# Kernel tuning notes

Measured on AMD Instinct MI355X. Metric: run time of the kernel, lower is better.

The kernel has to match this reference:

```python
import jax, jax.numpy as jnp
import numpy as np

N, B, NPG = 65536, 512, 128      # total nodes, graphs, nodes per graph
E, EPG = 524288, 1024            # total edges, edges per graph
D, R, L = 64, 16, 3              # emb_dim, num relations, encoder layers
PHI = 0.1
EPS_VAR = 1e-5


def _mean_std(x):
    # torch.var is unbiased (ddof=1); keep last-dim stats per row
    m = jnp.mean(x, axis=-1, keepdims=True)
    s = jnp.sqrt(jnp.var(x, axis=-1, ddof=1, keepdims=True) + EPS_VAR)
    return m, s


def _rgcn_encode(feat, Wrel, Wself, b, src, dst, etype, edge_w):
    """L-layer relational GCN. Returns (last_h [N,D], repr [N,L,D])."""
    h = feat
    reps = []
    for l in range(L):
        hr = jnp.einsum('nd,rdk->nrk', h, Wrel[l])        # [N,R,D]
        msg = hr[src, etype]                               # [E,D] per-edge typed transform
        msg = msg * edge_w[:, None]
        agg = jax.ops.segment_sum(msg, dst, num_segments=N)
        deg = jax.ops.segment_sum(edge_w, dst, num_segments=N)
        h = jax.nn.relu(h @ Wself[l] + agg / jnp.clip(deg, 1.0)[:, None] + b[l])
        reps.append(h)
    return h, jnp.stack(reps, axis=1)


def _pool(rep, node_gid):
    # mean_nodes over 'repr': graphs have fixed NPG nodes
    s = jax.ops.segment_sum(rep.reshape(N, L * D), node_gid, num_segments=B)
    return (s / NPG).reshape(B, L, D)


def full_forward(feat, rel_feat, rel_proj_W, rel_proj_b, rgcn_Wrel, rgcn_Wself,
                 rgcn_b, enc_W_mean, enc_W_std, dec_Wh, dec_bh, dec_Wt, dec_bt,
                 dec_Wr, dec_br, fc_W, fc_b, eps,
                 src, dst, etype, aug_src, aug_dst, aug_etype, node_gid, rel_labels):
    ones_e = jnp.ones((E,), feat.dtype)
    # relation encoder + projection
    emb_rel = jax.nn.relu(rel_feat @ rel_proj_W + rel_proj_b)          # [R,D]
    # encode original and augmented graphs
    x, rep_g = _rgcn_encode(feat, rgcn_Wrel, rgcn_Wself, rgcn_b, src, dst, etype, ones_e)
    g_out = _pool(rep_g, node_gid)
    aug_x, rep_aug = _rgcn_encode(feat, rgcn_Wrel, rgcn_Wself, rgcn_b, aug_src, aug_dst, aug_etype, ones_e)
    aug_g_out = _pool(rep_aug, node_gid)
    # AdaIn style transfer (args.interp == False)
    mc, sc = _mean_std(x)
    ms, ss = _mean_std(aug_x)
    style_applied = ss * ((x - mc) / sc) + ms
    # VAE reparameterization
    z_mean = style_applied @ enc_W_mean
    z_std = style_applied @ enc_W_std
    z = z_mean + jnp.sqrt(jnp.exp(z_std)) * eps
    # decoder: edge-level DistMult scoring -> edge mask
    head_e = jax.nn.relu(z[src] @ dec_Wh + dec_bh)                     # [E,D]
    tail_e = jax.nn.relu(z[dst] @ dec_Wt + dec_bt)
    rel_e = jax.nn.relu(emb_rel[etype] @ dec_Wr + dec_br)
    logit = jnp.sum(head_e * rel_e * tail_e, axis=-1)                  # [E]
    mask = (logit >= 0.5).astype(feat.dtype)
    # root edge (edge_ids(0,1)) = first edge of each graph, forced kept
    mask = mask.at[jnp.arange(B) * EPG].set(1.0)
    # re-encode reconstructed (masked) graph with original features
    x_recon, rep_recon = _rgcn_encode(feat, rgcn_Wrel, rgcn_Wself, rgcn_b, src, dst, etype, mask)
    recon_g_out = _pool(rep_recon, node_gid)
    # head node (id==1) = node 0 of each graph; tail (id==2) = node 1
    head_ids = jnp.arange(B) * NPG
    tail_ids = head_ids + 1
    g_rep = jnp.concatenate([
        recon_g_out.reshape(B, L * D),
        rep_recon[head_ids].reshape(B, L * D),
        rep_recon[tail_ids].reshape(B, L * D),
        emb_rel[rel_labels],
    ], axis=1)                                                          # [B, 3*L*D + D]
    output = g_rep @ fc_W + fc_b                                        # [B,1]
    # reconstruction + style losses, summed over layers
    mse_per_layer = jnp.mean((rep_recon - rep_g) ** 2, axis=(0, 2))     # [L]
    mr, sr = _mean_std(rep_recon.transpose(1, 0, 2))                    # [L,N,1]
    mg, sg = _mean_std(rep_g.transpose(1, 0, 2))
    style_per_layer = jnp.mean((mr - mg) ** 2, axis=(1, 2)) + jnp.mean((sr - sg) ** 2, axis=(1, 2))
    loss = jnp.sum(mse_per_layer) + PHI * jnp.sum(style_per_layer)
    return output, g_out, aug_g_out, loss


def setup_inputs() -> dict:
    key = jax.random.key(0)
    ks = jax.random.split(key, 28)
    egid = jnp.arange(E, dtype=jnp.int32) // EPG
    node_gid = jnp.arange(N, dtype=jnp.int32) // NPG
    mk_edges = lambda k1, k2: (egid * NPG + jax.random.randint(k1, (E,), 0, NPG, jnp.int32),
                               egid * NPG + jax.random.randint(k2, (E,), 0, NPG, jnp.int32))
    src, dst = mk_edges(ks[0], ks[1])
    aug_src, aug_dst = mk_edges(ks[2], ks[3])
    g = lambda i, shape, s=0.05: (jax.random.normal(ks[i], shape, jnp.float32) * s)
    return {
        'feat': g(4, (N, D), 1.0),
        'rel_feat': g(5, (R, 64), 1.0),
        'rel_proj_W': g(6, (64, D)),
        'rel_proj_b': jnp.zeros((D,), jnp.float32),
        'rgcn_Wrel': g(7, (L, R, D, D)),
        'rgcn_Wself': g(8, (L, D, D)),
        'rgcn_b': jnp.zeros((L, D), jnp.float32),
        'enc_W_mean': g(9, (D, D)),
        'enc_W_std': g(10, (D, D)),
        'dec_Wh': g(11, (D, D), 0.1),
        'dec_bh': jnp.zeros((D,), jnp.float32),
        'dec_Wt': g(12, (D, D), 0.1),
        'dec_bt': jnp.zeros((D,), jnp.float32),
        'dec_Wr': g(13, (D, D), 0.1),
        'dec_br': jnp.zeros((D,), jnp.float32),
        'fc_W': g(14, (3 * L * D + D, 1)),
        'fc_b': jnp.zeros((1,), jnp.float32),
        'eps': g(15, (N, D), 1.0),
        'src': src, 'dst': dst,
        'etype': jax.random.randint(ks[16], (E,), 0, R, jnp.int32),
        'aug_src': aug_src, 'aug_dst': aug_dst,
        'aug_etype': jax.random.randint(ks[17], (E,), 0, R, jnp.int32),
        'node_gid': node_gid,
        'rel_labels': jax.random.randint(ks[18], (B,), 0, R, jnp.int32),
    }


def reference(feat, rel_feat, rel_proj_W, rel_proj_b, rgcn_Wrel, rgcn_Wself,
              rgcn_b, enc_W_mean, enc_W_std, dec_Wh, dec_bh, dec_Wt, dec_bt,
              dec_Wr, dec_br, fc_W, fc_b, eps,
              src, dst, etype, aug_src, aug_dst, aug_etype, node_gid, rel_labels):
    return full_forward(feat, rel_feat, rel_proj_W, rel_proj_b, rgcn_Wrel, rgcn_Wself,
                        rgcn_b, enc_W_mean, enc_W_std, dec_Wh, dec_bh, dec_Wt, dec_bt,
                        dec_Wr, dec_br, fc_W, fc_b, eps,
                        src, dst, etype, aug_src, aug_dst, aug_etype, node_gid, rel_labels)
```

## Files before the change

### kernel.cpp

```cpp
#include <hip/hip_runtime.h>
#include <hip/hip_bf16.h>

typedef __attribute__((ext_vector_type(8))) short bf16x8;
typedef __attribute__((ext_vector_type(4))) float f32x4;

#define NPG  128
#define EPG  1024
#define BG   512
#define NT   512
#define NW   8
#define PHI  0.1f
#define EPSV 1e-5f
#define SB   72
#define SF   65

#define OUT_G    512
#define OUT_AUG  98816
#define OUT_LOSS 197120
#define WS_EMB   0
#define WS_RELE  1024
#define WS_REPG  2048

__device__ __forceinline__ unsigned short f2bf(float x) {
  __hip_bfloat16 h = __float2bfloat16(x);
  return *reinterpret_cast<unsigned short*>(&h);
}
__device__ __forceinline__ float bf2f(unsigned short u) {
  __hip_bfloat16 h = *reinterpret_cast<__hip_bfloat16*>(&u);
  return __bfloat162float(h);
}
__device__ __forceinline__ void split_write(unsigned short* hh, unsigned short* hl,
                                            int idx, float x) {
  unsigned short hi = f2bf(x);
  hh[idx] = hi;
  hl[idx] = f2bf(x - bf2f(hi));
}

#define LOAD_BF(Wp, ctn, ks, bhv, blv)                                         \
  {                                                                            \
    bf16x8 h_, l_;                                                             \
    _Pragma("unroll") for (int j_ = 0; j_ < 8; j_++) {                         \
      float w_ = (Wp)[((ks) * 32 + kg * 8 + j_) * 64 + (ctn) * 16 + n];        \
      unsigned short hi_ = f2bf(w_);                                           \
      h_[j_] = (short)hi_;                                                     \
      l_[j_] = (short)f2bf(w_ - bf2f(hi_));                                    \
    }                                                                          \
    bhv = h_;                                                                  \
    blv = l_;                                                                  \
  }

__device__ __forceinline__ f32x4 mfma3(bf16x8 a0h, bf16x8 a1h, bf16x8 a0l, bf16x8 a1l,
                                       bf16x8 b0h, bf16x8 b1h, bf16x8 b0l, bf16x8 b1l,
                                       f32x4 acc) {
  acc = __builtin_amdgcn_mfma_f32_16x16x32_bf16(a0h, b0h, acc, 0, 0, 0);
  acc = __builtin_amdgcn_mfma_f32_16x16x32_bf16(a1h, b1h, acc, 0, 0, 0);
  acc = __builtin_amdgcn_mfma_f32_16x16x32_bf16(a0h, b0l, acc, 0, 0, 0);
  acc = __builtin_amdgcn_mfma_f32_16x16x32_bf16(a1h, b1l, acc, 0, 0, 0);
  acc = __builtin_amdgcn_mfma_f32_16x16x32_bf16(a0l, b0h, acc, 0, 0, 0);
  acc = __builtin_amdgcn_mfma_f32_16x16x32_bf16(a1l, b1h, acc, 0, 0, 0);
  return acc;
}

__global__ __launch_bounds__(256) void k_prologue(
    const float* __restrict__ rel_feat, const float* __restrict__ rpW,
    const float* __restrict__ rpb, const float* __restrict__ dWr,
    const float* __restrict__ dbr, float* __restrict__ ws, float* __restrict__ out) {
  __shared__ float emb[1024];
  int tid = threadIdx.x;
  for (int idx = tid; idx < 1024; idx += 256) {
    int r = idx >> 6, j = idx & 63;
    float s = rpb[j];
    for (int k = 0; k < 64; k++) s = fmaf(rel_feat[r * 64 + k], rpW[k * 64 + j], s);
    s = fmaxf(s, 0.f);
    emb[idx] = s;
    ws[WS_EMB + idx] = s;
  }
  __syncthreads();
  for (int idx = tid; idx < 1024; idx += 256) {
    int r = idx >> 6, j = idx & 63;
    float s = dbr[j];
    for (int k = 0; k < 64; k++) s = fmaf(emb[r * 64 + k], dWr[k * 64 + j], s);
    ws[WS_RELE + idx] = fmaxf(s, 0.f);
  }
  if (tid == 0) out[OUT_LOSS] = 0.f;
}

__device__ void build_elist(unsigned* elist, int* cnt, int* offs, int* asg, int* wload,
                            float* dinv, const unsigned* maskbits, int useMask,
                            const int* __restrict__ et_a, const int* __restrict__ src_a,
                            const int* __restrict__ dst_a, int ge, int gn, int tid) {
  if (tid < 16) cnt[tid] = 0;
  if (tid >= 128 && tid < 256) dinv[tid - 128] = 0.f;
  __syncthreads();
  for (int i = tid; i < EPG; i += NT) {
    int keep = useMask ? (int)((maskbits[i >> 5] >> (i & 31)) & 1u) : 1;
    if (keep) {
      atomicAdd(&cnt[et_a[ge + i]], 1);
      atomicAdd(&dinv[dst_a[ge + i] - gn], 1.f);
    }
  }
  __syncthreads();
  if (tid == 0) {
    int o = 0;
    for (int r = 0; r < 16; r++) { offs[r] = o; o += (cnt[r] + 15) & ~15; }
    offs[16] = o;
    for (int w = 0; w < NW; w++) wload[w] = 0;
    unsigned used = 0;
    for (int s = 0; s < 16; s++) {
      int best = 0, bc = -1;
      for (int r = 0; r < 16; r++)
        if (!((used >> r) & 1) && cnt[r] > bc) { bc = cnt[r]; best = r; }
      used |= 1u << best;
      int bw = 0;
      for (int w = 1; w < NW; w++) if (wload[w] < wload[bw]) bw = w;
      asg[best] = bw;
      wload[bw] += (bc + 15) & ~15;
    }
  }
  if (tid >= 128 && tid < 256) {
    int v = tid - 128;
    dinv[v] = 1.0f / fmaxf(dinv[v], 1.0f);
  }
  __syncthreads();
  int total = offs[16];
  for (int s = tid; s < total; s += NT) elist[s] = 128u;
  if (tid < 16) cnt[tid] = offs[tid];
  __syncthreads();
  for (int i = tid; i < EPG; i += NT) {
    int keep = useMask ? (int)((maskbits[i >> 5] >> (i & 31)) & 1u) : 1;
    if (keep) {
      int r = et_a[ge + i];
      int pos = atomicAdd(&cnt[r], 1);
      elist[pos] = ((unsigned)(src_a[ge + i] - gn) << 8) | (unsigned)(dst_a[ge + i] - gn);
    }
  }
  __syncthreads();
}

__device__ void rgcn_layer_mfma(unsigned short* hh, unsigned short* hl, float* hf32,
                                const float* dinv, const unsigned* elist,
                                const int* offs, const int* asg,
                                const float* __restrict__ Wl,
                                const float* __restrict__ Wsl,
                                const float* __restrict__ bl, int tid) {
  int lane = tid & 63, wave = tid >> 6;
  int n = lane & 15, kg = lane >> 4;
  for (int i = tid; i < NPG * SF; i += NT) hf32[i] = 0.f;
  __syncthreads();
  for (int r = 0; r < 16; r++) {
    if (asg[r] != wave) continue;
    int base = offs[r], end = offs[r + 1];
    if (base >= end) continue;
    const float* __restrict__ W = Wl + (r << 12);
#pragma unroll 1
    for (int ch = 0; ch < 2; ch++) {
      bf16x8 bh00, bh01, bl00, bl01, bh10, bh11, bl10, bl11;
      LOAD_BF(W, ch * 2 + 0, 0, bh00, bl00);
      LOAD_BF(W, ch * 2 + 0, 1, bh01, bl01);
      LOAD_BF(W, ch * 2 + 1, 0, bh10, bl10);
      LOAD_BF(W, ch * 2 + 1, 1, bh11, bl11);
      for (int tb = base; tb < end; tb += 16) {
        int srow = (int)(elist[tb + n] >> 8);
        const unsigned short* rh = hh + srow * SB;
        const unsigned short* rl = hl + srow * SB;
        bf16x8 a0h = *(const bf16x8*)(rh + kg * 8);
        bf16x8 a1h = *(const bf16x8*)(rh + 32 + kg * 8);
        bf16x8 a0l = *(const bf16x8*)(rl + kg * 8);
        bf16x8 a1l = *(const bf16x8*)(rl + 32 + kg * 8);
        f32x4 acc0 = {0.f, 0.f, 0.f, 0.f}, acc1 = {0.f, 0.f, 0.f, 0.f};
        acc0 = mfma3(a0h, a1h, a0l, a1l, bh00, bh01, bl00, bl01, acc0);
        acc1 = mfma3(a0h, a1h, a0l, a1l, bh10, bh11, bl10, bl11, acc1);
#pragma unroll
        for (int i = 0; i < 4; i++) {
          int dst = (int)(elist[tb + kg * 4 + i] & 255u);
          if (dst < 128) {
            float* hp = hf32 + dst * SF + ch * 32 + n;
            atomicAdd(hp, acc0[i]);
            atomicAdd(hp + 16, acc1[i]);
          }
        }
      }
    }
  }
  __syncthreads();
  {
    const unsigned short* rh = hh + (wave * 16 + n) * SB;
    const unsigned short* rl = hl + (wave * 16 + n) * SB;
    bf16x8 a0h = *(const bf16x8*)(rh + kg * 8);
    bf16x8 a1h = *(const bf16x8*)(rh + 32 + kg * 8);
    bf16x8 a0l = *(const bf16x8*)(rl + kg * 8);
    bf16x8 a1l = *(const bf16x8*)(rl + 32 + kg * 8);
#pragma unroll 1
    for (int ch = 0; ch < 2; ch++) {
      bf16x8 bh00, bh01, bl00, bl01, bh10, bh11, bl10, bl11;
      LOAD_BF(Wsl, ch * 2 + 0, 0, bh00, bl00);
      LOAD_BF(Wsl, ch * 2 + 0, 1, bh01, bl01);
      LOAD_BF(Wsl, ch * 2 + 1, 0, bh10, bl10);
      LOAD_BF(Wsl, ch * 2 + 1, 1, bh11, bl11);
      f32x4 acc0 = {0.f, 0.f, 0.f, 0.f}, acc1 = {0.f, 0.f, 0.f, 0.f};
      acc0 = mfma3(a0h, a1h, a0l, a1l, bh00, bh01, bl00, bl01, acc0);
      acc1 = mfma3(a0h, a1h, a0l, a1l, bh10, bh11, bl10, bl11, acc1);
#pragma unroll
      for (int i = 0; i < 4; i++) {
        int node = wave * 16 + kg * 4 + i;
        float di = dinv[node];
#pragma unroll
        for (int c = 0; c < 2; c++) {
          int col = (ch * 2 + c) * 16 + n;
          float a = c ? acc1[i] : acc0[i];
          float v = a + hf32[node * SF + col] * di + bl[col];
          v = fmaxf(v, 0.f);
          hf32[node * SF + col] = v;
          split_write(hh, hl, node * SB + col, v);
        }
      }
    }
  }
  __syncthreads();
}

__device__ void dense_mfma(const unsigned short* ah, const unsigned short* al,
                           float* hf32, unsigned short* oh, unsigned short* ol,
                           const float* __restrict__ W, const float* __restrict__ bias,
                           int mode, const float* __restrict__ epsbuf, int gn, int tid) {
  int lane = tid & 63, wave = tid >> 6;
  int n = lane & 15, kg = lane >> 4;
  const unsigned short* rh = ah + (wave * 16 + n) * SB;
  const unsigned short* rl = al + (wave * 16 + n) * SB;
  bf16x8 a0h = *(const bf16x8*)(rh + kg * 8);
  bf16x8 a1h = *(const bf16x8*)(rh + 32 + kg * 8);
  bf16x8 a0l = *(const bf16x8*)(rl + kg * 8);
  bf16x8 a1l = *(const bf16x8*)(rl + 32 + kg * 8);
#pragma unroll 1
  for (int ch = 0; ch < 2; ch++) {
    bf16x8 bh00, bh01, bl00, bl01, bh10, bh11, bl10, bl11;
    LOAD_BF(W, ch * 2 + 0, 0, bh00, bl00);
    LOAD_BF(W, ch * 2 + 0, 1, bh01, bl01);
    LOAD_BF(W, ch * 2 + 1, 0, bh10, bl10);
    LOAD_BF(W, ch * 2 + 1, 1, bh11, bl11);
    f32x4 acc0 = {0.f, 0.f, 0.f, 0.f}, acc1 = {0.f, 0.f, 0.f, 0.f};
    acc0 = mfma3(a0h, a1h, a0l, a1l, bh00, bh01, bl00, bl01, acc0);
    acc1 = mfma3(a0h, a1h, a0l, a1l, bh10, bh11, bl10, bl11, acc1);
#pragma unroll
    for (int i = 0; i < 4; i++) {
      int node = wave * 16 + kg * 4 + i;
#pragma unroll
      for (int c = 0; c < 2; c++) {
        int col = (ch * 2 + c) * 16 + n;
        float a = c ? acc1[i] : acc0[i];
        if (mode == 0) {
          hf32[node * SF + col] = a;
        } else if (mode == 2) {
          hf32[node * SF + col] += sqrtf(expf(a)) * epsbuf[(gn + node) * 64 + col];
        } else {
          a = fmaxf(a + bias[col], 0.f);
          if (oh) split_write(oh, ol, node * SB + col, a);
          else hf32[node * SF + col] = a;
        }
      }
    }
  }
  __syncthreads();
}

__device__ void pool_sf(const float* hf32, float* red, float* dst, int tid) {
  int j = tid & 63, grp = tid >> 6;
  float s = 0.f;
  for (int v = grp * 16; v < grp * 16 + 16; v++) s += hf32[v * SF + j];
  red[tid] = s;
  __syncthreads();
  if (tid < 64) {
    float t = 0.f;
#pragma unroll
    for (int w = 0; w < NW; w++) t += red[w * 64 + tid];
    dst[tid] = t * (1.f / 128.f);
  }
  __syncthreads();
}

__global__ __launch_bounds__(NT, 2) void k_mega(
    const float* __restrict__ feat, const float* __restrict__ Wrel,
    const float* __restrict__ Wself, const float* __restrict__ bvec,
    const float* __restrict__ encWm, const float* __restrict__ encWs,
    const float* __restrict__ decWh, const float* __restrict__ dbh,
    const float* __restrict__ decWt, const float* __restrict__ dbt,
    const float* __restrict__ fcW, const float* __restrict__ fcb,
    const float* __restrict__ epsbuf,
    const int* __restrict__ srcA, const int* __restrict__ dstA, const int* __restrict__ etA,
    const int* __restrict__ asrcA, const int* __restrict__ adstA, const int* __restrict__ aetA,
    const int* __restrict__ rel_labels, float* __restrict__ ws, float* __restrict__ out) {
  __shared__ __align__(16) unsigned short hh[NPG * SB];
  __shared__ __align__(16) unsigned short hl[NPG * SB];
  __shared__ __align__(16) float hf32[NPG * SF];
  __shared__ __align__(16) unsigned elist[1280];
  __shared__ float dinv[NPG];
  __shared__ float red[NT];
  __shared__ float ht[384];
  __shared__ float rgout[192];
  __shared__ unsigned maskbits[EPG / 32];
  __shared__ int cnt[16], offs[17], asg[16], wload[NW];

  int g = blockIdx.x, tid = threadIdx.x;
  int gn = g * NPG, ge = g * EPG;
  float* repg = ws + WS_REPG;

  build_elist(elist, cnt, offs, asg, wload, dinv, maskbits, 0, etA, srcA, dstA, ge, gn, tid);
  for (int i = tid; i < 8192; i += NT)
    split_write(hh, hl, (i >> 6) * SB + (i & 63), feat[gn * 64 + i]);
  __syncthreads();
  for (int l = 0; l < 3; l++) {
    rgcn_layer_mfma(hh, hl, hf32, dinv, elist, offs, asg, Wrel + l * 65536,
                    Wself + l * 4096, bvec + l * 64, tid);
    for (int i = tid; i < 8192; i += NT)
      repg[(gn + (i >> 6)) * 192 + l * 64 + (i & 63)] = hf32[(i >> 6) * SF + (i & 63)];
    pool_sf(hf32, red, out + OUT_G + g * 192 + l * 64, tid);
  }
  build_elist(elist, cnt, offs, asg, wload, dinv, maskbits, 0, aetA, asrcA, adstA, ge, gn, tid);
  for (int i = tid; i < 8192; i += NT)
    split_write(hh, hl, (i >> 6) * SB + (i & 63), feat[gn * 64 + i]);
  __syncthreads();
  for (int l = 0; l < 3; l++) {
    rgcn_layer_mfma(hh, hl, hf32, dinv, elist, offs, asg, Wrel + l * 65536,
                    Wself + l * 4096, bvec + l * 64, tid);
    pool_sf(hf32, red, out + OUT_AUG + g * 192 + l * 64, tid);
  }
  if (tid < NPG) {
    int v = tid;
    float t1 = 0.f, t2 = 0.f;
    for (int jj = 0; jj < 64; jj++) {
      int j = (v + jj) & 63;
      float y = hf32[v * SF + j];
      t1 += y; t2 += y * y;
    }
    float ms = t1 * (1.f / 64.f);
    red[v] = ms;
    red[NPG + v] = sqrtf((t2 - 64.f * ms * ms) * (1.f / 63.f) + EPSV);
  }
  __syncthreads();
  for (int i = tid; i < 8192; i += NT)
    hf32[(i >> 6) * SF + (i & 63)] = repg[(gn + (i >> 6)) * 192 + 128 + (i & 63)];
  __syncthreads();
  if (tid < NPG) {
    int v = tid;
    float s1 = 0.f, s2 = 0.f;
    for (int jj = 0; jj < 64; jj++) {
      int j = (v + jj) & 63;
      float x = hf32[v * SF + j];
      s1 += x; s2 += x * x;
    }
    float mc = s1 * (1.f / 64.f);
    float sc = sqrtf((s2 - 64.f * mc * mc) * (1.f / 63.f) + EPSV);
    float sca = red[NPG + v] / sc, ms = red[v];
    for (int jj = 0; jj < 64; jj++) {
      int j = (v + jj) & 63;
      hf32[v * SF + j] = (hf32[v * SF + j] - mc) * sca + ms;
    }
  }
  __syncthreads();
  for (int i = tid; i < 8192; i += NT)
    split_write(hh, hl, (i >> 6) * SB + (i & 63), hf32[(i >> 6) * SF + (i & 63)]);
  __syncthreads();
  dense_mfma(hh, hl, hf32, nullptr, nullptr, encWm, nullptr, 0, nullptr, gn, tid);
  dense_mfma(hh, hl, hf32, nullptr, nullptr, encWs, nullptr, 2, epsbuf, gn, tid);
  for (int i = tid; i < 8192; i += NT)
    split_write(hh, hl, (i >> 6) * SB + (i & 63), hf32[(i >> 6) * SF + (i & 63)]);
  __syncthreads();
  dense_mfma(hh, hl, hf32, nullptr, nullptr, decWt, dbt, 1, nullptr, gn, tid);
  dense_mfma(hh, hl, hf32, hh, hl, decWh, dbh, 1, nullptr, gn, tid);
  float* relEl = (float*)elist;
  for (int i = tid; i < 1024; i += NT) relEl[i] = ws[WS_RELE + i];
  for (int i = tid; i < EPG / 32; i += NT) maskbits[i] = 0u;
  __syncthreads();
  for (int i = tid; i < EPG; i += NT) {
    int s = srcA[ge + i] - gn, t = dstA[ge + i] - gn, r = etA[ge + i];
    int rot = (s + t) & 63;
    float lg = 0.f;
    for (int jj = 0; jj < 64; jj++) {
      int j = (rot + jj) & 63;
      float zhv = bf2f(hh[s * SB + j]) + bf2f(hl[s * SB + j]);
      lg = fmaf(zhv * hf32[t * SF + j], relEl[(r << 6) + j], lg);
    }
    if (lg >= 0.5f) atomicOr(&maskbits[i >> 5], 1u << (i & 31));
  }
  __syncthreads();
  if (tid == 0) maskbits[0] |= 1u;
  __syncthreads();
  build_elist(elist, cnt, offs, asg, wload, dinv, maskbits, 1, etA, srcA, dstA, ge, gn, tid);
  for (int i = tid; i < 8192; i += NT)
    split_write(hh, hl, (i >> 6) * SB + (i & 63), feat[gn * 64 + i]);
  __syncthreads();
  const float c1 = 1.0f / (65536.0f * 64.0f);
  const float c2 = PHI / 65536.0f;
  for (int l = 0; l < 3; l++) {
    rgcn_layer_mfma(hh, hl, hf32, dinv, elist, offs, asg, Wrel + l * 65536,
                    Wself + l * 4096, bvec + l * 64, tid);
    pool_sf(hf32, red, rgout + l * 64, tid);
    if (tid < 128)
      ht[(l * 2 + (tid >> 6)) * 64 + (tid & 63)] = hf32[(tid >> 6) * SF + (tid & 63)];
    {
      int v = tid >> 2, q = tid & 3;
      const float* gp = repg + (gn + v) * 192 + l * 64 + q * 16;
      const float* hp = hf32 + v * SF + q * 16;
      float mse = 0.f, a1 = 0.f, a2 = 0.f, b1 = 0.f, b2 = 0.f;
#pragma unroll
      for (int u = 0; u < 16; u++) {
        float rc = hp[u];
        float gg = gp[u];
        float d = rc - gg;
        mse += d * d; a1 += rc; a2 += rc * rc; b1 += gg; b2 += gg * gg;
      }
#pragma unroll
      for (int m = 1; m < 4; m <<= 1) {
        mse += __shfl_xor(mse, m); a1 += __shfl_xor(a1, m); a2 += __shfl_xor(a2, m);
        b1 += __shfl_xor(b1, m); b2 += __shfl_xor(b2, m);
      }
      if (q == 0) {
        float mr = a1 * (1.f / 64.f), mg = b1 * (1.f / 64.f);
        float sr = sqrtf((a2 - 64.f * mr * mr) * (1.f / 63.f) + EPSV);
        float sg = sqrtf((b2 - 64.f * mg * mg) * (1.f / 63.f) + EPSV);
        float style = (mr - mg) * (mr - mg) + (sr - sg) * (sr - sg);
        red[v] = mse * c1 + style * c2;
      }
    }
    __syncthreads();
    if (tid < 64) {
      float x = red[tid] + red[tid + 64];
#pragma unroll
      for (int o = 32; o > 0; o >>= 1) x += __shfl_down(x, o);
      if (tid == 0) atomicAdd(&out[OUT_LOSS], x);
    }
    __syncthreads();
  }
  if (tid < 64) {
    int rl = rel_labels[g];
    const float* emb = ws + WS_EMB + rl * 64;
    float s = 0.f;
    for (int p = 0; p < 10; p++) {
      int i = p * 64 + tid;
      float gr;
      if (i < 192) gr = rgout[i];
      else if (i < 384) { int i2 = i - 192; gr = ht[((i2 >> 6) * 2 + 0) * 64 + (i2 & 63)]; }
      else if (i < 576) { int i2 = i - 384; gr = ht[((i2 >> 6) * 2 + 1) * 64 + (i2 & 63)]; }
      else gr = emb[i - 576];
      s = fmaf(gr, fcW[i], s);
    }
#pragma unroll
    for (int o = 32; o > 0; o >>= 1) s += __shfl_down(s, o);
    if (tid == 0) out[g] = s + fcb[0];
  }
}

extern "C" void kernel_launch(void* const* d_in, const int* in_sizes, int n_in,
                              void* d_out, int out_size, void* d_ws, size_t ws_size,
                              hipStream_t stream) {
  const float* feat     = (const float*)d_in[0];
  const float* rel_feat = (const float*)d_in[1];
  const float* rpW      = (const float*)d_in[2];
  const float* rpb      = (const float*)d_in[3];
  const float* Wrel     = (const float*)d_in[4];
  const float* Wself    = (const float*)d_in[5];
  const float* bvec     = (const float*)d_in[6];
  const float* encWm    = (const float*)d_in[7];
  const float* encWs    = (const float*)d_in[8];
  const float* decWh    = (const float*)d_in[9];
  const float* dbh      = (const float*)d_in[10];
  const float* decWt    = (const float*)d_in[11];
  const float* dbt      = (const float*)d_in[12];
  const float* decWr    = (const float*)d_in[13];
  const float* dbr      = (const float*)d_in[14];
  const float* fcW      = (const float*)d_in[15];
  const float* fcb      = (const float*)d_in[16];
  const float* epsb     = (const float*)d_in[17];
  const int* srcA  = (const int*)d_in[18];
  const int* dstA  = (const int*)d_in[19];
  const int* etA   = (const int*)d_in[20];
  const int* asrcA = (const int*)d_in[21];
  const int* adstA = (const int*)d_in[22];
  const int* aetA  = (const int*)d_in[23];
  const int* rel_labels = (const int*)d_in[25];
  float* out = (float*)d_out;
  float* ws  = (float*)d_ws;

  k_prologue<<<1, 256, 0, stream>>>(rel_feat, rpW, rpb, decWr, dbr, ws, out);
  k_mega<<<BG, NT, 0, stream>>>(feat, Wrel, Wself, bvec, encWm, encWs, decWh, dbh,
                                decWt, dbt, fcW, fcb, epsb, srcA, dstA, etA,
                                asrcA, adstA, aetA, rel_labels, ws, out);
}
```

Before: 1.528 ms.

## Double block to 1024 threads and split RGCN work into relation-half items

The per-graph mega-kernel now runs 16 waves per block instead of 8. Relation scatter work is split into 32 items (relation × output-column half), assigned greedily across waves. Self-transform and dense GEMMs give each wave a 16-row by 32-column tile, with an extra barrier when the output overwrites the input. This aims to raise per-graph parallelism and latency hiding. The cost is more barrier overhead, a launch_bounds occupancy request of 4 that may pressure registers, and more idle threads in sections that are still gated to 512 threads.

Result: slower. 1.750 ms (+14.6%).

```diff
diff --git a/kernel.cpp b/kernel.cpp
--- a/kernel.cpp
+++ b/kernel.cpp
@@ -7,8 +7,8 @@
 #define NPG  128
 #define EPG  1024
 #define BG   512
-#define NT   512
-#define NW   8
+#define NT   1024
+#define NW   16
 #define PHI  0.1f
 #define EPSV 1e-5f
 #define SB   72
@@ -85,7 +85,7 @@
   if (tid == 0) out[OUT_LOSS] = 0.f;
 }
 
-__device__ void build_elist(unsigned* elist, int* cnt, int* offs, int* asg, int* wload,
+__device__ void build_elist(unsigned* elist, int* cnt, int* offs, int* asg2, int* wload,
                             float* dinv, const unsigned* maskbits, int useMask,
                             const int* __restrict__ et_a, const int* __restrict__ src_a,
                             const int* __restrict__ dst_a, int ge, int gn, int tid) {
@@ -106,15 +106,18 @@
     offs[16] = o;
     for (int w = 0; w < NW; w++) wload[w] = 0;
     unsigned used = 0;
-    for (int s = 0; s < 16; s++) {
+    for (int s = 0; s < 32; s++) {
       int best = 0, bc = -1;
-      for (int r = 0; r < 16; r++)
-        if (!((used >> r) & 1) && cnt[r] > bc) { bc = cnt[r]; best = r; }
+      for (int it = 0; it < 32; it++)
+        if (!((used >> it) & 1)) {
+          int sz = (cnt[it >> 1] + 15) & ~15;
+          if (sz > bc) { bc = sz; best = it; }
+        }
       used |= 1u << best;
       int bw = 0;
       for (int w = 1; w < NW; w++) if (wload[w] < wload[bw]) bw = w;
-      asg[best] = bw;
-      wload[bw] += (bc + 15) & ~15;
+      asg2[best] = bw;
+      wload[bw] += bc;
     }
   }
   if (tid >= 128 && tid < 256) {
@@ -139,7 +142,7 @@
 
 __device__ void rgcn_layer_mfma(unsigned short* hh, unsigned short* hl, float* hf32,
                                 const float* dinv, const unsigned* elist,
-                                const int* offs, const int* asg,
+                                const int* offs, const int* asg2,
                                 const float* __restrict__ Wl,
                                 const float* __restrict__ Wsl,
                                 const float* __restrict__ bl, int tid) {
@@ -147,116 +150,114 @@
   int n = lane & 15, kg = lane >> 4;
   for (int i = tid; i < NPG * SF; i += NT) hf32[i] = 0.f;
   __syncthreads();
-  for (int r = 0; r < 16; r++) {
-    if (asg[r] != wave) continue;
+  for (int item = 0; item < 32; item++) {
+    if (asg2[item] != wave) continue;
+    int r = item >> 1, ch = item & 1;
     int base = offs[r], end = offs[r + 1];
     if (base >= end) continue;
     const float* __restrict__ W = Wl + (r << 12);
-#pragma unroll 1
-    for (int ch = 0; ch < 2; ch++) {
-      bf16x8 bh00, bh01, bl00, bl01, bh10, bh11, bl10, bl11;
-      LOAD_BF(W, ch * 2 + 0, 0, bh00, bl00);
-      LOAD_BF(W, ch * 2 + 0, 1, bh01, bl01);
-      LOAD_BF(W, ch * 2 + 1, 0, bh10, bl10);
-      LOAD_BF(W, ch * 2 + 1, 1, bh11, bl11);
-      for (int tb = base; tb < end; tb += 16) {
-        int srow = (int)(elist[tb + n] >> 8);
-        const unsigned short* rh = hh + srow * SB;
-        const unsigned short* rl = hl + srow * SB;
-        bf16x8 a0h = *(const bf16x8*)(rh + kg * 8);
-        bf16x8 a1h = *(const bf16x8*)(rh + 32 + kg * 8);
-        bf16x8 a0l = *(const bf16x8*)(rl + kg * 8);
-        bf16x8 a1l = *(const bf16x8*)(rl + 32 + kg * 8);
-        f32x4 acc0 = {0.f, 0.f, 0.f, 0.f}, acc1 = {0.f, 0.f, 0.f, 0.f};
-        acc0 = mfma3(a0h, a1h, a0l, a1l, bh00, bh01, bl00, bl01, acc0);
-        acc1 = mfma3(a0h, a1h, a0l, a1l, bh10, bh11, bl10, bl11, acc1);
-#pragma unroll
-        for (int i = 0; i < 4; i++) {
-          int dst = (int)(elist[tb + kg * 4 + i] & 255u);
-          if (dst < 128) {
-            float* hp = hf32 + dst * SF + ch * 32 + n;
-            atomicAdd(hp, acc0[i]);
-            atomicAdd(hp + 16, acc1[i]);
-          }
-        }
-      }
-    }
-  }
-  __syncthreads();
-  {
-    const unsigned short* rh = hh + (wave * 16 + n) * SB;
-    const unsigned short* rl = hl + (wave * 16 + n) * SB;
-    bf16x8 a0h = *(const bf16x8*)(rh + kg * 8);
-    bf16x8 a1h = *(const bf16x8*)(rh + 32 + kg * 8);
-    bf16x8 a0l = *(const bf16x8*)(rl + kg * 8);
-    bf16x8 a1l = *(const bf16x8*)(rl + 32 + kg * 8);
-#pragma unroll 1
-    for (int ch = 0; ch < 2; ch++) {
-      bf16x8 bh00, bh01, bl00, bl01, bh10, bh11, bl10, bl11;
-      LOAD_BF(Wsl, ch * 2 + 0, 0, bh00, bl00);
-      LOAD_BF(Wsl, ch * 2 + 0, 1, bh01, bl01);
-      LOAD_BF(Wsl, ch * 2 + 1, 0, bh10, bl10);
-      LOAD_BF(Wsl, ch * 2 + 1, 1, bh11, bl11);
-      f32x4 acc0 = {0.f, 0.f, 0.f, 0.f}, acc1 = {0.f, 0.f, 0.f, 0.f};
-      acc0 = mfma3(a0h, a1h, a0l, a1l, bh00, bh01, bl00, bl01, acc0);
-      acc1 = mfma3(a0h, a1h, a0l, a1l, bh10, bh11, bl10, bl11, acc1);
-#pragma unroll
-      for (int i = 0; i < 4; i++) {
-        int node = wave * 16 + kg * 4 + i;
-        float di = dinv[node];
-#pragma unroll
-        for (int c = 0; c < 2; c++) {
-          int col = (ch * 2 + c) * 16 + n;
-          float a = c ? acc1[i] : acc0[i];
-          float v = a + hf32[node * SF + col] * di + bl[col];
-          v = fmaxf(v, 0.f);
-          hf32[node * SF + col] = v;
-          split_write(hh, hl, node * SB + col, v);
-        }
-      }
-    }
-  }
-  __syncthreads();
-}
-
-__device__ void dense_mfma(const unsigned short* ah, const unsigned short* al,
-                           float* hf32, unsigned short* oh, unsigned short* ol,
-                           const float* __restrict__ W, const float* __restrict__ bias,
-                           int mode, const float* __restrict__ epsbuf, int gn, int tid) {
-  int lane = tid & 63, wave = tid >> 6;
-  int n = lane & 15, kg = lane >> 4;
-  const unsigned short* rh = ah + (wave * 16 + n) * SB;
-  const unsigned short* rl = al + (wave * 16 + n) * SB;
-  bf16x8 a0h = *(const bf16x8*)(rh + kg * 8);
-  bf16x8 a1h = *(const bf16x8*)(rh + 32 + kg * 8);
-  bf16x8 a0l = *(const bf16x8*)(rl + kg * 8);
-  bf16x8 a1l = *(const bf16x8*)(rl + 32 + kg * 8);
-#pragma unroll 1
-  for (int ch = 0; ch < 2; ch++) {
     bf16x8 bh00, bh01, bl00, bl01, bh10, bh11, bl10, bl11;
     LOAD_BF(W, ch * 2 + 0, 0, bh00, bl00);
     LOAD_BF(W, ch * 2 + 0, 1, bh01, bl01);
     LOAD_BF(W, ch * 2 + 1, 0, bh10, bl10);
     LOAD_BF(W, ch * 2 + 1, 1, bh11, bl11);
+    for (int tb = base; tb < end; tb += 16) {
+      unsigned e = elist[tb + n];
+      int srow = (int)(e >> 8);
+      const unsigned short* rh = hh + srow * SB;
+      const unsigned short* rl = hl + srow * SB;
+      bf16x8 a0h = *(const bf16x8*)(rh + kg * 8);
+      bf16x8 a1h = *(const bf16x8*)(rh + 32 + kg * 8);
+      bf16x8 a0l = *(const bf16x8*)(rl + kg * 8);
+      bf16x8 a1l = *(const bf16x8*)(rl + 32 + kg * 8);
+      f32x4 acc0 = {0.f, 0.f, 0.f, 0.f}, acc1 = {0.f, 0.f, 0.f, 0.f};
+      acc0 = mfma3(a0h, a1h, a0l, a1l, bh00, bh01, bl00, bl01, acc0);
+      acc1 = mfma3(a0h, a1h, a0l, a1l, bh10, bh11, bl10, bl11, acc1);
+#pragma unroll
+      for (int i = 0; i < 4; i++) {
+        int dst = (int)(elist[tb + kg * 4 + i] & 255u);
+        if (dst < 128) {
+          float* hp = hf32 + dst * SF + ch * 32 + n;
+          atomicAdd(hp, acc0[i]);
+          atomicAdd(hp + 16, acc1[i]);
+        }
+      }
+    }
+  }
+  __syncthreads();
+  {
+    int w2 = wave >> 1, chs = wave & 1;
+    const unsigned short* rh = hh + (w2 * 16 + n) * SB;
+    const unsigned short* rl = hl + (w2 * 16 + n) * SB;
+    bf16x8 a0h = *(const bf16x8*)(rh + kg * 8);
+    bf16x8 a1h = *(const bf16x8*)(rh + 32 + kg * 8);
+    bf16x8 a0l = *(const bf16x8*)(rl + kg * 8);
+    bf16x8 a1l = *(const bf16x8*)(rl + 32 + kg * 8);
+    __syncthreads();
+    bf16x8 bh00, bh01, bl00, bl01, bh10, bh11, bl10, bl11;
+    LOAD_BF(Wsl, chs * 2 + 0, 0, bh00, bl00);
+    LOAD_BF(Wsl, chs * 2 + 0, 1, bh01, bl01);
+    LOAD_BF(Wsl, chs * 2 + 1, 0, bh10, bl10);
+    LOAD_BF(Wsl, chs * 2 + 1, 1, bh11, bl11);
     f32x4 acc0 = {0.f, 0.f, 0.f, 0.f}, acc1 = {0.f, 0.f, 0.f, 0.f};
     acc0 = mfma3(a0h, a1h, a0l, a1l, bh00, bh01, bl00, bl01, acc0);
     acc1 = mfma3(a0h, a1h, a0l, a1l, bh10, bh11, bl10, bl11, acc1);
 #pragma unroll
     for (int i = 0; i < 4; i++) {
-      int node = wave * 16 + kg * 4 + i;
+      int node = w2 * 16 + kg * 4 + i;
+      float di = dinv[node];
 #pragma unroll
       for (int c = 0; c < 2; c++) {
-        int col = (ch * 2 + c) * 16 + n;
+        int col = (chs * 2 + c) * 16 + n;
         float a = c ? acc1[i] : acc0[i];
-        if (mode == 0) {
-          hf32[node * SF + col] = a;
-        } else if (mode == 2) {
-          hf32[node * SF + col] += sqrtf(expf(a)) * epsbuf[(gn + node) * 64 + col];
-        } else {
-          a = fmaxf(a + bias[col], 0.f);
-          if (oh) split_write(oh, ol, node * SB + col, a);
-          else hf32[node * SF + col] = a;
-        }
+        float v = a + hf32[node * SF + col] * di + bl[col];
+        v = fmaxf(v, 0.f);
+        hf32[node * SF + col] = v;
+        split_write(hh, hl, node * SB + col, v);
+      }
+    }
+  }
+  __syncthreads();
+}
+
+__device__ void dense_mfma(const unsigned short* ah, const unsigned short* al,
+                           float* hf32, unsigned short* oh, unsigned short* ol,
+                           const float* __restrict__ W, const float* __restrict__ bias,
+                           int mode, const float* __restrict__ epsbuf, int gn, int tid,
+                           int inplace) {
+  int lane = tid & 63, wave = tid >> 6;
+  int n = lane & 15, kg = lane >> 4;
+  int w2 = wave >> 1, chs = wave & 1;
+  const unsigned short* rh = ah + (w2 * 16 + n) * SB;
+  const unsigned short* rl = al + (w2 * 16 + n) * SB;
+  bf16x8 a0h = *(const bf16x8*)(rh + kg * 8);
+  bf16x8 a1h = *(const bf16x8*)(rh + 32 + kg * 8);
+  bf16x8 a0l = *(const bf16x8*)(rl + kg * 8);
+  bf16x8 a1l = *(const bf16x8*)(rl + 32 + kg * 8);
+  if (inplace) __syncthreads();
+  bf16x8 bh00, bh01, bl00, bl01, bh10, bh11, bl10, bl11;
+  LOAD_BF(W, chs * 2 + 0, 0, bh00, bl00);
+  LOAD_BF(W, chs * 2 + 0, 1, bh01, bl01);
+  LOAD_BF(W, chs * 2 + 1, 0, bh10, bl10);
+  LOAD_BF(W, chs * 2 + 1, 1, bh11, bl11);
+  f32x4 acc0 = {0.f, 0.f, 0.f, 0.f}, acc1 = {0.f, 0.f, 0.f, 0.f};
+  acc0 = mfma3(a0h, a1h, a0l, a1l, bh00, bh01, bl00, bl01, acc0);
+  acc1 = mfma3(a0h, a1h, a0l, a1l, bh10, bh11, bl10, bl11, acc1);
+#pragma unroll
+  for (int i = 0; i < 4; i++) {
+    int node = w2 * 16 + kg * 4 + i;
+#pragma unroll
+    for (int c = 0; c < 2; c++) {
+      int col = (chs * 2 + c) * 16 + n;
+      float a = c ? acc1[i] : acc0[i];
+      if (mode == 0) {
+        hf32[node * SF + col] = a;
+      } else if (mode == 2) {
+        hf32[node * SF + col] += sqrtf(expf(a)) * epsbuf[(gn + node) * 64 + col];
+      } else {
+        a = fmaxf(a + bias[col], 0.f);
+        if (oh) split_write(oh, ol, node * SB + col, a);
+        else hf32[node * SF + col] = a;
       }
     }
   }
@@ -264,21 +265,23 @@
 }
 
 __device__ void pool_sf(const float* hf32, float* red, float* dst, int tid) {
-  int j = tid & 63, grp = tid >> 6;
-  float s = 0.f;
-  for (int v = grp * 16; v < grp * 16 + 16; v++) s += hf32[v * SF + j];
-  red[tid] = s;
+  if (tid < 512) {
+    int j = tid & 63, grp = tid >> 6;
+    float s = 0.f;
+    for (int v = grp * 16; v < grp * 16 + 16; v++) s += hf32[v * SF + j];
+    red[tid] = s;
+  }
   __syncthreads();
   if (tid < 64) {
     float t = 0.f;
 #pragma unroll
-    for (int w = 0; w < NW; w++) t += red[w * 64 + tid];
+    for (int w = 0; w < 8; w++) t += red[w * 64 + tid];
     dst[tid] = t * (1.f / 128.f);
   }
   __syncthreads();
 }
 
-__global__ __launch_bounds__(NT, 2) void k_mega(
+__global__ __launch_bounds__(NT, 4) void k_mega(
     const float* __restrict__ feat, const float* __restrict__ Wrel,
     const float* __restrict__ Wself, const float* __restrict__ bvec,
     const float* __restrict__ encWm, const float* __restrict__ encWs,
@@ -292,35 +295,35 @@
   __shared__ __align__(16) unsigned short hh[NPG * SB];
   __shared__ __align__(16) unsigned short hl[NPG * SB];
   __shared__ __align__(16) float hf32[NPG * SF];
-  __shared__ __align__(16) unsigned elist[1280];
+  __shared__ __align__(16) unsigned elist[1264];
   __shared__ float dinv[NPG];
-  __shared__ float red[NT];
+  __shared__ float red[512];
   __shared__ float ht[384];
   __shared__ float rgout[192];
   __shared__ unsigned maskbits[EPG / 32];
-  __shared__ int cnt[16], offs[17], asg[16], wload[NW];
+  __shared__ int cnt[16], offs[17], asg2[32], wload[NW];
 
   int g = blockIdx.x, tid = threadIdx.x;
   int gn = g * NPG, ge = g * EPG;
   float* repg = ws + WS_REPG;
 
-  build_elist(elist, cnt, offs, asg, wload, dinv, maskbits, 0, etA, srcA, dstA, ge, gn, tid);
+  build_elist(elist, cnt, offs, asg2, wload, dinv, maskbits, 0, etA, srcA, dstA, ge, gn, tid);
   for (int i = tid; i < 8192; i += NT)
     split_write(hh, hl, (i >> 6) * SB + (i & 63), feat[gn * 64 + i]);
   __syncthreads();
   for (int l = 0; l < 3; l++) {
-    rgcn_layer_mfma(hh, hl, hf32, dinv, elist, offs, asg, Wrel + l * 65536,
+    rgcn_layer_mfma(hh, hl, hf32, dinv, elist, offs, asg2, Wrel + l * 65536,
                     Wself + l * 4096, bvec + l * 64, tid);
     for (int i = tid; i < 8192; i += NT)
       repg[(gn + (i >> 6)) * 192 + l * 64 + (i & 63)] = hf32[(i >> 6) * SF + (i & 63)];
     pool_sf(hf32, red, out + OUT_G + g * 192 + l * 64, tid);
   }
-  build_elist(elist, cnt, offs, asg, wload, dinv, maskbits, 0, aetA, asrcA, adstA, ge, gn, tid);
+  build_elist(elist, cnt, offs, asg2, wload, dinv, maskbits, 0, aetA, asrcA, adstA, ge, gn, tid);
   for (int i = tid; i < 8192; i += NT)
     split_write(hh, hl, (i >> 6) * SB + (i & 63), feat[gn * 64 + i]);
   __syncthreads();
   for (int l = 0; l < 3; l++) {
-    rgcn_layer_mfma(hh, hl, hf32, dinv, elist, offs, asg, Wrel + l * 65536,
+    rgcn_layer_mfma(hh, hl, hf32, dinv, elist, offs, asg2, Wrel + l * 65536,
                     Wself + l * 4096, bvec + l * 64, tid);
     pool_sf(hf32, red, out + OUT_AUG + g * 192 + l * 64, tid);
   }
@@ -360,13 +363,13 @@
   for (int i = tid; i < 8192; i += NT)
     split_write(hh, hl, (i >> 6) * SB + (i & 63), hf32[(i >> 6) * SF + (i & 63)]);
   __syncthreads();
-  dense_mfma(hh, hl, hf32, nullptr, nullptr, encWm, nullptr, 0, nullptr, gn, tid);
-  dense_mfma(hh, hl, hf32, nullptr, nullptr, encWs, nullptr, 2, epsbuf, gn, tid);
+  dense_mfma(hh, hl, hf32, nullptr, nullptr, encWm, nullptr, 0, nullptr, gn, tid, 0);
+  dense_mfma(hh, hl, hf32, nullptr, nullptr, encWs, nullptr, 2, epsbuf, gn, tid, 0);
   for (int i = tid; i < 8192; i += NT)
     split_write(hh, hl, (i >> 6) * SB + (i & 63), hf32[(i >> 6) * SF + (i & 63)]);
   __syncthreads();
-  dense_mfma(hh, hl, hf32, nullptr, nullptr, decWt, dbt, 1, nullptr, gn, tid);
-  dense_mfma(hh, hl, hf32, hh, hl, decWh, dbh, 1, nullptr, gn, tid);
+  dense_mfma(hh, hl, hf32, nullptr, nullptr, decWt, dbt, 1, nullptr, gn, tid, 0);
+  dense_mfma(hh, hl, hf32, hh, hl, decWh, dbh, 1, nullptr, gn, tid, 1);
   float* relEl = (float*)elist;
   for (int i = tid; i < 1024; i += NT) relEl[i] = ws[WS_RELE + i];
   for (int i = tid; i < EPG / 32; i += NT) maskbits[i] = 0u;
@@ -385,19 +388,19 @@
   __syncthreads();
   if (tid == 0) maskbits[0] |= 1u;
   __syncthreads();
-  build_elist(elist, cnt, offs, asg, wload, dinv, maskbits, 1, etA, srcA, dstA, ge, gn, tid);
+  build_elist(elist, cnt, offs, asg2, wload, dinv, maskbits, 1, etA, srcA, dstA, ge, gn, tid);
   for (int i = tid; i < 8192; i += NT)
     split_write(hh, hl, (i >> 6) * SB + (i & 63), feat[gn * 64 + i]);
   __syncthreads();
   const float c1 = 1.0f / (65536.0f * 64.0f);
   const float c2 = PHI / 65536.0f;
   for (int l = 0; l < 3; l++) {
-    rgcn_layer_mfma(hh, hl, hf32, dinv, elist, offs, asg, Wrel + l * 65536,
+    rgcn_layer_mfma(hh, hl, hf32, dinv, elist, offs, asg2, Wrel + l * 65536,
                     Wself + l * 4096, bvec + l * 64, tid);
     pool_sf(hf32, red, rgout + l * 64, tid);
     if (tid < 128)
       ht[(l * 2 + (tid >> 6)) * 64 + (tid & 63)] = hf32[(tid >> 6) * SF + (tid & 63)];
-    {
+    if (tid < 512) {
       int v = tid >> 2, q = tid & 3;
       const float* gp = repg + (gn + v) * 192 + l * 64 + q * 16;
       const float* hp = hf32 + v * SF + q * 16;
```

## Use static relation-to-wave assignment and deterministic per-block loss reduction

Applied to the files above, without the earlier changes.

Replaces the serial greedy load-balancing of relations onto waves, computed by one thread, with a fixed round-robin mapping (wave w handles relations w and w+8). Instead of every block doing a global atomicAdd into the loss, each block writes a partial sum to workspace and a new single-block finishing kernel reduces the 512 partials. This removes serial thread-0 work and global atomic contention, but adds a kernel launch and may leave waves unevenly loaded when relation counts are skewed.

Measured after the change: 1.584 ms. 3.7% more time.

```diff
diff --git a/kernel.cpp b/kernel.cpp
--- a/kernel.cpp
+++ b/kernel.cpp
@@ -19,7 +19,8 @@
 #define OUT_LOSS 197120
 #define WS_EMB   0
 #define WS_RELE  1024
-#define WS_REPG  2048
+#define WS_LOSSP 2048
+#define WS_REPG  4096
 
 __device__ __forceinline__ unsigned short f2bf(float x) {
   __hip_bfloat16 h = __float2bfloat16(x);
@@ -64,7 +65,7 @@
 __global__ __launch_bounds__(256) void k_prologue(
     const float* __restrict__ rel_feat, const float* __restrict__ rpW,
     const float* __restrict__ rpb, const float* __restrict__ dWr,
-    const float* __restrict__ dbr, float* __restrict__ ws, float* __restrict__ out) {
+    const float* __restrict__ dbr, float* __restrict__ ws) {
   __shared__ float emb[1024];
   int tid = threadIdx.x;
   for (int idx = tid; idx < 1024; idx += 256) {
@@ -82,11 +83,27 @@
     for (int k = 0; k < 64; k++) s = fmaf(emb[r * 64 + k], dWr[k * 64 + j], s);
     ws[WS_RELE + idx] = fmaxf(s, 0.f);
   }
-  if (tid == 0) out[OUT_LOSS] = 0.f;
-}
-
-__device__ void build_elist(unsigned* elist, int* cnt, int* offs, int* asg, int* wload,
-                            float* dinv, const unsigned* maskbits, int useMask,
+}
+
+__global__ __launch_bounds__(512) void k_fin(const float* __restrict__ ws,
+                                             float* __restrict__ out) {
+  __shared__ float red[8];
+  int tid = threadIdx.x;
+  float x = ws[WS_LOSSP + tid];
+#pragma unroll
+  for (int o = 32; o > 0; o >>= 1) x += __shfl_down(x, o);
+  if ((tid & 63) == 0) red[tid >> 6] = x;
+  __syncthreads();
+  if (tid == 0) {
+    float s = 0.f;
+#pragma unroll
+    for (int w = 0; w < 8; w++) s += red[w];
+    out[OUT_LOSS] = s;
+  }
+}
+
+__device__ void build_elist(unsigned* elist, int* cnt, int* offs, float* dinv,
+                            const unsigned* maskbits, int useMask,
                             const int* __restrict__ et_a, const int* __restrict__ src_a,
                             const int* __restrict__ dst_a, int ge, int gn, int tid) {
   if (tid < 16) cnt[tid] = 0;
@@ -102,20 +119,9 @@
   __syncthreads();
   if (tid == 0) {
     int o = 0;
+#pragma unroll
     for (int r = 0; r < 16; r++) { offs[r] = o; o += (cnt[r] + 15) & ~15; }
     offs[16] = o;
-    for (int w = 0; w < NW; w++) wload[w] = 0;
-    unsigned used = 0;
-    for (int s = 0; s < 16; s++) {
-      int best = 0, bc = -1;
-      for (int r = 0; r < 16; r++)
-        if (!((used >> r) & 1) && cnt[r] > bc) { bc = cnt[r]; best = r; }
-      used |= 1u << best;
-      int bw = 0;
-      for (int w = 1; w < NW; w++) if (wload[w] < wload[bw]) bw = w;
-      asg[best] = bw;
-      wload[bw] += (bc + 15) & ~15;
-    }
   }
   if (tid >= 128 && tid < 256) {
     int v = tid - 128;
@@ -139,7 +145,7 @@
 
 __device__ void rgcn_layer_mfma(unsigned short* hh, unsigned short* hl, float* hf32,
                                 const float* dinv, const unsigned* elist,
-                                const int* offs, const int* asg,
+                                const int* offs,
                                 const float* __restrict__ Wl,
                                 const float* __restrict__ Wsl,
                                 const float* __restrict__ bl, int tid) {
@@ -147,8 +153,7 @@
   int n = lane & 15, kg = lane >> 4;
   for (int i = tid; i < NPG * SF; i += NT) hf32[i] = 0.f;
   __syncthreads();
-  for (int r = 0; r < 16; r++) {
-    if (asg[r] != wave) continue;
+  for (int r = wave; r < 16; r += NW) {
     int base = offs[r], end = offs[r + 1];
     if (base >= end) continue;
     const float* __restrict__ W = Wl + (r << 12);
@@ -160,7 +165,8 @@
       LOAD_BF(W, ch * 2 + 1, 0, bh10, bl10);
       LOAD_BF(W, ch * 2 + 1, 1, bh11, bl11);
       for (int tb = base; tb < end; tb += 16) {
-        int srow = (int)(elist[tb + n] >> 8);
+        unsigned e = elist[tb + n];
+        int srow = (int)(e >> 8);
         const unsigned short* rh = hh + srow * SB;
         const unsigned short* rl = hl + srow * SB;
         bf16x8 a0h = *(const bf16x8*)(rh + kg * 8);
@@ -298,29 +304,30 @@
   __shared__ float ht[384];
   __shared__ float rgout[192];
   __shared__ unsigned maskbits[EPG / 32];
-  __shared__ int cnt[16], offs[17], asg[16], wload[NW];
+  __shared__ int cnt[16], offs[17];
 
   int g = blockIdx.x, tid = threadIdx.x;
   int gn = g * NPG, ge = g * EPG;
   float* repg = ws + WS_REPG;
-
-  build_elist(elist, cnt, offs, asg, wload, dinv, maskbits, 0, etA, srcA, dstA, ge, gn, tid);
+  float loss_acc = 0.f;
+
+  build_elist(elist, cnt, offs, dinv, maskbits, 0, etA, srcA, dstA, ge, gn, tid);
   for (int i = tid; i < 8192; i += NT)
     split_write(hh, hl, (i >> 6) * SB + (i & 63), feat[gn * 64 + i]);
   __syncthreads();
   for (int l = 0; l < 3; l++) {
-    rgcn_layer_mfma(hh, hl, hf32, dinv, elist, offs, asg, Wrel + l * 65536,
+    rgcn_layer_mfma(hh, hl, hf32, dinv, elist, offs, Wrel + l * 65536,
                     Wself + l * 4096, bvec + l * 64, tid);
     for (int i = tid; i < 8192; i += NT)
       repg[(gn + (i >> 6)) * 192 + l * 64 + (i & 63)] = hf32[(i >> 6) * SF + (i & 63)];
     pool_sf(hf32, red, out + OUT_G + g * 192 + l * 64, tid);
   }
-  build_elist(elist, cnt, offs, asg, wload, dinv, maskbits, 0, aetA, asrcA, adstA, ge, gn, tid);
+  build_elist(elist, cnt, offs, dinv, maskbits, 0, aetA, asrcA, adstA, ge, gn, tid);
   for (int i = tid; i < 8192; i += NT)
     split_write(hh, hl, (i >> 6) * SB + (i & 63), feat[gn * 64 + i]);
   __syncthreads();
   for (int l = 0; l < 3; l++) {
-    rgcn_layer_mfma(hh, hl, hf32, dinv, elist, offs, asg, Wrel + l * 65536,
+    rgcn_layer_mfma(hh, hl, hf32, dinv, elist, offs, Wrel + l * 65536,
                     Wself + l * 4096, bvec + l * 64, tid);
     pool_sf(hf32, red, out + OUT_AUG + g * 192 + l * 64, tid);
   }
@@ -385,14 +392,14 @@
   __syncthreads();
   if (tid == 0) maskbits[0] |= 1u;
   __syncthreads();
-  build_elist(elist, cnt, offs, asg, wload, dinv, maskbits, 1, etA, srcA, dstA, ge, gn, tid);
+  build_elist(elist, cnt, offs, dinv, maskbits, 1, etA, srcA, dstA, ge, gn, tid);
   for (int i = tid; i < 8192; i += NT)
     split_write(hh, hl, (i >> 6) * SB + (i & 63), feat[gn * 64 + i]);
   __syncthreads();
   const float c1 = 1.0f / (65536.0f * 64.0f);
   const float c2 = PHI / 65536.0f;
   for (int l = 0; l < 3; l++) {
-    rgcn_layer_mfma(hh, hl, hf32, dinv, elist, offs, asg, Wrel + l * 65536,
+    rgcn_layer_mfma(hh, hl, hf32, dinv, elist, offs, Wrel + l * 65536,
                     Wself + l * 4096, bvec + l * 64, tid);
     pool_sf(hf32, red, rgout + l * 64, tid);
     if (tid < 128)
@@ -427,10 +434,11 @@
       float x = red[tid] + red[tid + 64];
 #pragma unroll
       for (int o = 32; o > 0; o >>= 1) x += __shfl_down(x, o);
-      if (tid == 0) atomicAdd(&out[OUT_LOSS], x);
+      if (tid == 0) loss_acc += x;
     }
     __syncthreads();
   }
+  if (tid == 0) ws[WS_LOSSP + g] = loss_acc;
   if (tid < 64) {
     int rl = rel_labels[g];
     const float* emb = ws + WS_EMB + rl * 64;
@@ -481,8 +489,9 @@
   float* out = (float*)d_out;
   float* ws  = (float*)d_ws;
 
-  k_prologue<<<1, 256, 0, stream>>>(rel_feat, rpW, rpb, decWr, dbr, ws, out);
+  k_prologue<<<1, 256, 0, stream>>>(rel_feat, rpW, rpb, decWr, dbr, ws);
   k_mega<<<BG, NT, 0, stream>>>(feat, Wrel, Wself, bvec, encWm, encWs, decWh, dbh,
                                 decWt, dbt, fcW, fcb, epsb, srcA, dstA, etA,
                                 asrcA, adstA, aetA, rel_labels, ws, out);
-}
+  k_fin<<<1, 512, 0, stream>>>(ws, out);
+}
```
